# Kernel tuning notes

Measured on AMD Instinct MI355X. Metric: run time of the kernel, lower is better.

The kernel has to match this reference:

```python
import jax, jax.numpy as jnp
import numpy as np

N, E, B = 100000, 1600000, 64
IN, HID, OUT, ED = 64, 128, 128, 2
K, ALPHA = 16, 0.1
LN_EPS = 1e-5


def setup_inputs() -> dict:
    key = jax.random.key(0)
    ks = jax.random.split(key, 24)
    def gl(k, shape, fan_in):
        return jax.random.uniform(k, shape, jnp.float32, -1.0, 1.0) / np.sqrt(fan_in)
    inp = {
        "x": jax.random.normal(ks[0], (N, IN), jnp.float32),
        "edge_index": jax.random.randint(ks[1], (2, E), 0, N, jnp.int64),
        "batch": jnp.sort(jax.random.randint(ks[2], (N,), 0, B, jnp.int64)),
        "edge_attr": jax.random.normal(ks[3], (E, ED), jnp.float32),
        # conv1: edge lin (ED->IN) + mlp (IN->HID->HID)
        "We1": gl(ks[4], (ED, IN), ED), "be1": jnp.zeros((IN,)),
        "W1a": gl(ks[5], (IN, HID), IN), "b1a": jnp.zeros((HID,)),
        "W1b": gl(ks[6], (HID, HID), HID), "b1b": jnp.zeros((HID,)),
        "g1": jnp.ones((HID,)), "bn1": jnp.zeros((HID,)),
        # conv2: edge lin (ED->HID) + mlp (HID->OUT->OUT)
        "We2": gl(ks[7], (ED, HID), ED), "be2": jnp.zeros((HID,)),
        "W2a": gl(ks[8], (HID, OUT), HID), "b2a": jnp.zeros((OUT,)),
        "W2b": gl(ks[9], (OUT, OUT), OUT), "b2b": jnp.zeros((OUT,)),
        "g2": jnp.ones((OUT,)), "bn2": jnp.zeros((OUT,)),
        # gate nn (OUT -> OUT//2 -> 1)
        "Wg1": gl(ks[10], (OUT, OUT // 2), OUT), "bg1": jnp.zeros((OUT // 2,)),
        "Wg2": gl(ks[11], (OUT // 2, 1), OUT // 2), "bg2": jnp.zeros((1,)),
    }
    return inp


def _gelu(x):
    return jax.nn.gelu(x, approximate=False)


def _layernorm(x, g, b):
    mu = jnp.mean(x, axis=-1, keepdims=True)
    var = jnp.mean(jnp.square(x - mu), axis=-1, keepdims=True)
    return (x - mu) * jax.lax.rsqrt(var + LN_EPS) * g + b


def _gine(x, src, dst, edge_attr, We, be, W1, b1, W2, b2):
    # message: ReLU(x_j + lin(edge_attr)), aggregated by sum at dst; eps=0
    m = jax.nn.relu(x[src] + edge_attr @ We + be)          # [E, d]
    agg = jax.ops.segment_sum(m, dst, num_segments=N)      # [N, d]
    h = x + agg
    return _gelu(h @ W1 + b1) @ W2 + b2


def _appnp(x, src, dst):
    # gcn_norm with self-loops: deg_i = 1 + in-degree
    deg = jax.ops.segment_sum(jnp.ones((E,), x.dtype), dst, num_segments=N) + 1.0
    dis = jax.lax.rsqrt(deg)
    w = dis[src] * dis[dst]            # [E]
    selfw = 1.0 / deg                  # [N]
    def step(i, h):
        prop = jax.ops.segment_sum(w[:, None] * h[src], dst, num_segments=N) \
               + selfw[:, None] * h
        return (1.0 - ALPHA) * prop + ALPHA * x
    return jax.lax.fori_loop(0, K, step, x)


def reference(x, edge_index, batch, edge_attr,
              We1, be1, W1a, b1a, W1b, b1b, g1, bn1,
              We2, be2, W2a, b2a, W2b, b2b, g2, bn2,
              Wg1, bg1, Wg2, bg2):
    src, dst = edge_index[0], edge_index[1]
    h = _gine(x, src, dst, edge_attr, We1, be1, W1a, b1a, W1b, b1b)
    h = _layernorm(_gelu(h), g1, bn1)
    # dropout is identity in eval
    h = _gine(h, src, dst, edge_attr, We2, be2, W2a, b2a, W2b, b2b)
    h = _layernorm(h, g2, bn2)
    h = _appnp(h, src, dst)
    # attentional aggregation: per-graph softmax over gate scores
    gate = (_gelu(h @ Wg1 + bg1) @ Wg2 + bg2)[:, 0]        # [N]
    m = jax.ops.segment_max(gate, batch, num_segments=B)    # [B]
    e = jnp.exp(gate - m[batch])
    s = jax.ops.segment_sum(e, batch, num_segments=B)
    a = e / s[batch]
    g = jax.ops.segment_sum(a[:, None] * h, batch, num_segments=B)  # [B, OUT]
    return h, g
```

## Files before the change

### kernel.cpp

```cpp
#include <hip/hip_runtime.h>
#include <math.h>

#define N_NODES 100000
#define N_EDGES 1600000
#define N_B 64
#define D_IN 64
#define D_HID 128
#define D_OUT 128
#define K_ITER 16
#define LN_EPS 1e-5f

typedef short s8v __attribute__((ext_vector_type(8)));
typedef float f4v __attribute__((ext_vector_type(4)));

__device__ __forceinline__ float gelu_f(float x) {
    return 0.5f * x * (1.0f + erff(0.70710678118654752440f * x));
}

__device__ __forceinline__ float ubx(unsigned u) { return __uint_as_float(u << 16); }
__device__ __forceinline__ float uby(unsigned u) { return __uint_as_float(u & 0xffff0000u); }

__device__ __forceinline__ unsigned short bf_rne(float x) {
    unsigned u = __float_as_uint(x);
    u += 0x7fffu + ((u >> 16) & 1u);
    return (unsigned short)(u >> 16);
}
__device__ __forceinline__ float bf_f(unsigned short s) {
    return __uint_as_float(((unsigned)s) << 16);
}
__device__ __forceinline__ unsigned pack_bf2(float a, float b) {
    return (unsigned)bf_rne(a) | (((unsigned)bf_rne(b)) << 16);
}


__global__ __launch_bounds__(256) void hist_kernel(const int* __restrict__ dst, int* __restrict__ counts) {
    int e = blockIdx.x * 256 + threadIdx.x;
    if (e < N_EDGES) atomicAdd(&counts[dst[e]], 1);
}

__global__ __launch_bounds__(256) void deg_kernel(const int* __restrict__ counts,
                                                  float* __restrict__ dis, float* __restrict__ selfw,
                                                  float* __restrict__ rsq) {
    int i = blockIdx.x * 256 + threadIdx.x;
    if (i < N_NODES) {
        float d = (float)(counts[i] + 1);
        dis[i] = 1.0f / sqrtf(d);
        selfw[i] = 1.0f / d;
        rsq[i] = sqrtf(d);
    }
}

__global__ __launch_bounds__(1024) void scan1(const int* __restrict__ counts, int* __restrict__ rp,
                                              int* __restrict__ bsum) {
    __shared__ int tmp[1024];
    int t = threadIdx.x;
    int idx = blockIdx.x * 1024 + t;
    int v = (idx < N_NODES) ? counts[idx] : 0;
    tmp[t] = v;
    __syncthreads();
    for (int o = 1; o < 1024; o <<= 1) {
        int add = (t >= o) ? tmp[t - o] : 0;
        __syncthreads();
        tmp[t] += add;
        __syncthreads();
    }
    if (idx < N_NODES) rp[idx] = tmp[t] - v;
    if (t == 1023) bsum[blockIdx.x] = tmp[t];
}

__global__ void scan2(int* bsum, int nb) {
    if (threadIdx.x == 0 && blockIdx.x == 0) {
        int acc = 0;
        for (int i = 0; i < nb; i++) { int v = bsum[i]; bsum[i] = acc; acc += v; }
    }
}

__global__ __launch_bounds__(1024) void scan3(int* __restrict__ rp, const int* __restrict__ bsum,
                                              int* __restrict__ cursor) {
    int t = threadIdx.x;
    int idx = blockIdx.x * 1024 + t;
    if (idx < N_NODES) {
        int v = rp[idx] + bsum[blockIdx.x];
        rp[idx] = v;
        cursor[idx] = v;
    }
    if (idx == 0) rp[N_NODES] = N_EDGES;
}

__global__ __launch_bounds__(256) void scatter_kernel(const int* __restrict__ src, const int* __restrict__ dst,
                                                      const float* __restrict__ ea,
                                                      int* __restrict__ cursor, int4* __restrict__ edata) {
    int e = blockIdx.x * 256 + threadIdx.x;
    if (e >= N_EDGES) return;
    int s = src[e], d = dst[e];
    int pos = atomicAdd(&cursor[d], 1);
    float2 e2 = ((const float2*)ea)[e];
    int4 v;
    v.x = s;
    v.y = __float_as_int(e2.x);
    v.z = __float_as_int(e2.y);
    v.w = 0;
    edata[pos] = v;
}

__global__ __launch_bounds__(256) void split_kernel(const int4* __restrict__ edata, int* __restrict__ esrc) {
    int e = blockIdx.x * 256 + threadIdx.x;
    if (e < N_EDGES) esrc[e] = edata[e].x;
}

__global__ __launch_bounds__(256) void x_to_bf(const float4* __restrict__ x4, uint2* __restrict__ xb2) {
    int i = blockIdx.x * 256 + threadIdx.x;
    if (i < N_NODES * 16) {
        float4 v = x4[i];
        uint2 o;
        o.x = pack_bf2(v.x, v.y);
        o.y = pack_bf2(v.z, v.w);
        xb2[i] = o;
    }
}


__global__ __launch_bounds__(256) void conv1_gather(const float* __restrict__ x,
                                                    const unsigned short* __restrict__ xb,
                                                    const int* __restrict__ rp,
                                                    const int4* __restrict__ edata,
                                                    const float* __restrict__ We1, const float* __restrict__ be1,
                                                    float* __restrict__ out) {
    int gw = (blockIdx.x * 256 + threadIdx.x) >> 6;
    if (gw >= N_NODES) return;
    int lane = threadIdx.x & 63;
    float w0 = We1[lane], w1 = We1[64 + lane], bb = be1[lane];
    float acc = x[(size_t)gw * 64 + lane];
    int j = rp[gw], jend = rp[gw + 1];
    for (; j + 8 <= jend; j += 8) {
        int4 e0 = edata[j], e1 = edata[j + 1], e2 = edata[j + 2], e3 = edata[j + 3];
        int4 e4 = edata[j + 4], e5 = edata[j + 5], e6 = edata[j + 6], e7 = edata[j + 7];
        unsigned short v0 = xb[(size_t)e0.x * 64 + lane];
        unsigned short v1 = xb[(size_t)e1.x * 64 + lane];
        unsigned short v2 = xb[(size_t)e2.x * 64 + lane];
        unsigned short v3 = xb[(size_t)e3.x * 64 + lane];
        unsigned short v4 = xb[(size_t)e4.x * 64 + lane];
        unsigned short v5 = xb[(size_t)e5.x * 64 + lane];
        unsigned short v6 = xb[(size_t)e6.x * 64 + lane];
        unsigned short v7 = xb[(size_t)e7.x * 64 + lane];
        acc += fmaxf(bf_f(v0) + __int_as_float(e0.y) * w0 + __int_as_float(e0.z) * w1 + bb, 0.0f);
        acc += fmaxf(bf_f(v1) + __int_as_float(e1.y) * w0 + __int_as_float(e1.z) * w1 + bb, 0.0f);
        acc += fmaxf(bf_f(v2) + __int_as_float(e2.y) * w0 + __int_as_float(e2.z) * w1 + bb, 0.0f);
        acc += fmaxf(bf_f(v3) + __int_as_float(e3.y) * w0 + __int_as_float(e3.z) * w1 + bb, 0.0f);
        acc += fmaxf(bf_f(v4) + __int_as_float(e4.y) * w0 + __int_as_float(e4.z) * w1 + bb, 0.0f);
        acc += fmaxf(bf_f(v5) + __int_as_float(e5.y) * w0 + __int_as_float(e5.z) * w1 + bb, 0.0f);
        acc += fmaxf(bf_f(v6) + __int_as_float(e6.y) * w0 + __int_as_float(e6.z) * w1 + bb, 0.0f);
        acc += fmaxf(bf_f(v7) + __int_as_float(e7.y) * w0 + __int_as_float(e7.z) * w1 + bb, 0.0f);
    }
    for (; j < jend; j++) {
        int4 e = edata[j];
        unsigned short v = xb[(size_t)e.x * 64 + lane];
        acc += fmaxf(bf_f(v) + __int_as_float(e.y) * w0 + __int_as_float(e.z) * w1 + bb, 0.0f);
    }
    out[(size_t)gw * 64 + lane] = acc;
}

__global__ __launch_bounds__(256) void conv2_gather(const float* __restrict__ h1f, const unsigned* __restrict__ h1b,
                                                    const int* __restrict__ rp,
                                                    const int4* __restrict__ edata,
                                                    const float* __restrict__ We2, const float* __restrict__ be2,
                                                    float* __restrict__ out) {
    int gw = (blockIdx.x * 256 + threadIdx.x) >> 6;
    if (gw >= N_NODES) return;
    int lane = threadIdx.x & 63;
    int f0 = lane * 2;
    float w00 = We2[f0], w01 = We2[f0 + 1];
    float w10 = We2[128 + f0], w11 = We2[128 + f0 + 1];
    float b0 = be2[f0], b1 = be2[f0 + 1];
    float2 hc = ((const float2*)h1f)[(size_t)gw * 64 + lane];
    float a0 = hc.x, a1 = hc.y;
    int j = rp[gw], jend = rp[gw + 1];
    for (; j + 8 <= jend; j += 8) {
        int4 e0 = edata[j], e1 = edata[j + 1], e2 = edata[j + 2], e3 = edata[j + 3];
        int4 e4 = edata[j + 4], e5 = edata[j + 5], e6 = edata[j + 6], e7 = edata[j + 7];
        unsigned v0 = h1b[(size_t)e0.x * 64 + lane];
        unsigned v1 = h1b[(size_t)e1.x * 64 + lane];
        unsigned v2 = h1b[(size_t)e2.x * 64 + lane];
        unsigned v3 = h1b[(size_t)e3.x * 64 + lane];
        unsigned v4 = h1b[(size_t)e4.x * 64 + lane];
        unsigned v5 = h1b[(size_t)e5.x * 64 + lane];
        unsigned v6 = h1b[(size_t)e6.x * 64 + lane];
        unsigned v7 = h1b[(size_t)e7.x * 64 + lane];
        a0 += fmaxf(ubx(v0) + __int_as_float(e0.y) * w00 + __int_as_float(e0.z) * w10 + b0, 0.0f);
        a1 += fmaxf(uby(v0) + __int_as_float(e0.y) * w01 + __int_as_float(e0.z) * w11 + b1, 0.0f);
        a0 += fmaxf(ubx(v1) + __int_as_float(e1.y) * w00 + __int_as_float(e1.z) * w10 + b0, 0.0f);
        a1 += fmaxf(uby(v1) + __int_as_float(e1.y) * w01 + __int_as_float(e1.z) * w11 + b1, 0.0f);
        a0 += fmaxf(ubx(v2) + __int_as_float(e2.y) * w00 + __int_as_float(e2.z) * w10 + b0, 0.0f);
        a1 += fmaxf(uby(v2) + __int_as_float(e2.y) * w01 + __int_as_float(e2.z) * w11 + b1, 0.0f);
        a0 += fmaxf(ubx(v3) + __int_as_float(e3.y) * w00 + __int_as_float(e3.z) * w10 + b0, 0.0f);
        a1 += fmaxf(uby(v3) + __int_as_float(e3.y) * w01 + __int_as_float(e3.z) * w11 + b1, 0.0f);
        a0 += fmaxf(ubx(v4) + __int_as_float(e4.y) * w00 + __int_as_float(e4.z) * w10 + b0, 0.0f);
        a1 += fmaxf(uby(v4) + __int_as_float(e4.y) * w01 + __int_as_float(e4.z) * w11 + b1, 0.0f);
        a0 += fmaxf(ubx(v5) + __int_as_float(e5.y) * w00 + __int_as_float(e5.z) * w10 + b0, 0.0f);
        a1 += fmaxf(uby(v5) + __int_as_float(e5.y) * w01 + __int_as_float(e5.z) * w11 + b1, 0.0f);
        a0 += fmaxf(ubx(v6) + __int_as_float(e6.y) * w00 + __int_as_float(e6.z) * w10 + b0, 0.0f);
        a1 += fmaxf(uby(v6) + __int_as_float(e6.y) * w01 + __int_as_float(e6.z) * w11 + b1, 0.0f);
        a0 += fmaxf(ubx(v7) + __int_as_float(e7.y) * w00 + __int_as_float(e7.z) * w10 + b0, 0.0f);
        a1 += fmaxf(uby(v7) + __int_as_float(e7.y) * w01 + __int_as_float(e7.z) * w11 + b1, 0.0f);
    }
    for (; j < jend; j++) {
        int4 e = edata[j];
        unsigned v = h1b[(size_t)e.x * 64 + lane];
        a0 += fmaxf(ubx(v) + __int_as_float(e.y) * w00 + __int_as_float(e.z) * w10 + b0, 0.0f);
        a1 += fmaxf(uby(v) + __int_as_float(e.y) * w01 + __int_as_float(e.z) * w11 + b1, 0.0f);
    }
    out[(size_t)gw * 128 + f0] = a0;
    out[(size_t)gw * 128 + f0 + 1] = a1;
}


template <int Kd, bool GELU, bool LN, int OMODE, bool SCALE>
__global__ __launch_bounds__(256) void mlp_mfma(const float* __restrict__ A, const float* __restrict__ W,
                                                const float* __restrict__ bias, const float* __restrict__ g,
                                                const float* __restrict__ bn, float* __restrict__ outf,
                                                unsigned short* __restrict__ outb,
                                                const float* __restrict__ uscale) {
    __shared__ unsigned short sHi[8192];
    __shared__ unsigned short sLo[8192];
    int wave = threadIdx.x >> 6, lane = threadIdx.x & 63;
    int quad = lane >> 4, n = lane & 15;
    int rowA = blockIdx.x * 64 + wave * 16 + n;
    int rowAc = (rowA < N_NODES) ? rowA : 0;

    f4v acc[8];
    #pragma unroll
    for (int t = 0; t < 8; t++) acc[t] = (f4v){0.f, 0.f, 0.f, 0.f};

    for (int ph = 0; ph < Kd / 64; ph++) {
        __syncthreads();
        for (int idx = threadIdx.x; idx < 8192; idx += 256) {
            int k = idx >> 7, c = idx & 127;
            float v = W[(size_t)(ph * 64 + k) * 128 + c];
            unsigned short hi = bf_rne(v);
            unsigned short lo = bf_rne(v - bf_f(hi));
            int kk = k >> 5, q = (k >> 3) & 3, j = k & 7, t = c >> 4, nn = c & 15;
            int lidx = ((((kk * 4 + q) * 8 + t) * 16 + nn) << 3) + j;
            sHi[lidx] = hi;
            sLo[lidx] = lo;
        }
        __syncthreads();
        #pragma unroll
        for (int kk = 0; kk < 2; kk++) {
            int k0 = ph * 64 + kk * 32 + quad * 8;
            const float4* ap = (const float4*)(A + (size_t)rowAc * Kd + k0);
            float4 a0 = ap[0], a1 = ap[1];
            float av[8] = {a0.x, a0.y, a0.z, a0.w, a1.x, a1.y, a1.z, a1.w};
            s8v ahi, alo;
            #pragma unroll
            for (int j = 0; j < 8; j++) {
                unsigned short h = bf_rne(av[j]);
                ahi[j] = (short)h;
                alo[j] = (short)bf_rne(av[j] - bf_f(h));
            }
            int base = ((kk * 4 + quad) * 8) * 128;
            #pragma unroll
            for (int t = 0; t < 8; t++) {
                s8v bhi = *(const s8v*)&sHi[base + ((t * 16 + n) << 3)];
                s8v blo = *(const s8v*)&sLo[base + ((t * 16 + n) << 3)];
                acc[t] = __builtin_amdgcn_mfma_f32_16x16x32_bf16(ahi, bhi, acc[t], 0, 0, 0);
                acc[t] = __builtin_amdgcn_mfma_f32_16x16x32_bf16(ahi, blo, acc[t], 0, 0, 0);
                acc[t] = __builtin_amdgcn_mfma_f32_16x16x32_bf16(alo, bhi, acc[t], 0, 0, 0);
            }
        }
    }

    float bcol[8], gcol[8], bncol[8];
    #pragma unroll
    for (int t = 0; t < 8; t++) {
        bcol[t] = bias[t * 16 + n];
        if (LN) { gcol[t] = g[t * 16 + n]; bncol[t] = bn[t * 16 + n]; }
    }
    #pragma unroll
    for (int r = 0; r < 4; r++) {
        int row = blockIdx.x * 64 + wave * 16 + quad * 4 + r;
        float v[8];
        #pragma unroll
        for (int t = 0; t < 8; t++) {
            float x = acc[t][r] + bcol[t];
            v[t] = GELU ? gelu_f(x) : x;
        }
        if (LN) {
            float s = 0.f, q2 = 0.f;
            #pragma unroll
            for (int t = 0; t < 8; t++) { s += v[t]; q2 += v[t] * v[t]; }
            #pragma unroll
            for (int m = 1; m <= 8; m <<= 1) {
                s += __shfl_xor(s, m, 64);
                q2 += __shfl_xor(q2, m, 64);
            }
            float mu = s * (1.0f / 128.0f);
            float rs = rsqrtf(q2 * (1.0f / 128.0f) - mu * mu + LN_EPS);
            #pragma unroll
            for (int t = 0; t < 8; t++) v[t] = (v[t] - mu) * rs * gcol[t] + bncol[t];
        }
        if (row < N_NODES) {
            float us = SCALE ? uscale[row] : 1.0f;
            #pragma unroll
            for (int t = 0; t < 8; t++) {
                if (OMODE != 2) outf[(size_t)row * 128 + t * 16 + n] = v[t];
                if (OMODE >= 1) outb[(size_t)row * 128 + t * 16 + n] = bf_rne(SCALE ? v[t] * us : v[t]);
            }
        }
    }
}


__global__ __launch_bounds__(256) void gate_mfma(const float* __restrict__ h, const float* __restrict__ Wg1,
                                                 const float* __restrict__ bg1, const float* __restrict__ Wg2,
                                                 const float* __restrict__ bg2, float* __restrict__ gate) {
    __shared__ unsigned short sHi[8192];
    __shared__ unsigned short sLo[8192];
    int wave = threadIdx.x >> 6, lane = threadIdx.x & 63;
    int quad = lane >> 4, n = lane & 15;
    for (int idx = threadIdx.x; idx < 8192; idx += 256) {
        int k = idx >> 6, c = idx & 63;
        float v = Wg1[k * 64 + c];
        unsigned short hi = bf_rne(v);
        unsigned short lo = bf_rne(v - bf_f(hi));
        int kk = k >> 5, q = (k >> 3) & 3, j = k & 7, t = c >> 4, nn = c & 15;
        int lidx = ((((kk * 4 + q) * 4 + t) * 16 + nn) << 3) + j;
        sHi[lidx] = hi;
        sLo[lidx] = lo;
    }
    __syncthreads();
    int rowA = blockIdx.x * 64 + wave * 16 + n;
    int rowAc = (rowA < N_NODES) ? rowA : 0;
    f4v acc[4];
    #pragma unroll
    for (int t = 0; t < 4; t++) acc[t] = (f4v){0.f, 0.f, 0.f, 0.f};
    #pragma unroll
    for (int kk = 0; kk < 4; kk++) {
        const float4* ap = (const float4*)(h + (size_t)rowAc * 128 + kk * 32 + quad * 8);
        float4 a0 = ap[0], a1 = ap[1];
        float av[8] = {a0.x, a0.y, a0.z, a0.w, a1.x, a1.y, a1.z, a1.w};
        s8v ahi, alo;
        #pragma unroll
        for (int j = 0; j < 8; j++) {
            unsigned short hh = bf_rne(av[j]);
            ahi[j] = (short)hh;
            alo[j] = (short)bf_rne(av[j] - bf_f(hh));
        }
        int base = ((kk * 4 + quad) * 4) * 128;
        #pragma unroll
        for (int t = 0; t < 4; t++) {
            s8v bhi = *(const s8v*)&sHi[base + ((t * 16 + n) << 3)];
            s8v blo = *(const s8v*)&sLo[base + ((t * 16 + n) << 3)];
            acc[t] = __builtin_amdgcn_mfma_f32_16x16x32_bf16(ahi, bhi, acc[t], 0, 0, 0);
            acc[t] = __builtin_amdgcn_mfma_f32_16x16x32_bf16(ahi, blo, acc[t], 0, 0, 0);
            acc[t] = __builtin_amdgcn_mfma_f32_16x16x32_bf16(alo, bhi, acc[t], 0, 0, 0);
        }
    }
    float b2 = bg2[0];
    float bb[4], vv[4];
    #pragma unroll
    for (int t = 0; t < 4; t++) { bb[t] = bg1[t * 16 + n]; vv[t] = Wg2[t * 16 + n]; }
    #pragma unroll
    for (int r = 0; r < 4; r++) {
        int row = blockIdx.x * 64 + wave * 16 + quad * 4 + r;
        float val = 0.f;
        #pragma unroll
        for (int t = 0; t < 4; t++) val += gelu_f(acc[t][r] + bb[t]) * vv[t];
        #pragma unroll
        for (int m = 1; m <= 8; m <<= 1) val += __shfl_xor(val, m, 64);
        if (n == 0 && row < N_NODES) gate[row] = val + b2;
    }
}


template <bool LAST>
__global__ __launch_bounds__(256) void appnp_step_u(const unsigned* __restrict__ hin,
                                                    const unsigned* __restrict__ anchor,
                                                    unsigned* __restrict__ hout, float2* __restrict__ houtf,
                                                    const int* __restrict__ rp, const int* __restrict__ esrc,
                                                    const float* __restrict__ selfw,
                                                    const float* __restrict__ rsq) {
    int gw = (blockIdx.x * 256 + threadIdx.x) >> 6;
    if (gw >= N_NODES) return;
    int lane = threadIdx.x & 63;
    size_t idx = (size_t)gw * 64 + lane;
    unsigned hcp = hin[idx];
    float ax = ubx(hcp), ay = uby(hcp);
    int j = rp[gw], jend = rp[gw + 1];
    for (; j + 8 <= jend; j += 8) {
        int s0 = esrc[j],     s1 = esrc[j + 1], s2 = esrc[j + 2], s3 = esrc[j + 3];
        int s4 = esrc[j + 4], s5 = esrc[j + 5], s6 = esrc[j + 6], s7 = esrc[j + 7];
        unsigned v0 = hin[(size_t)s0 * 64 + lane];
        unsigned v1 = hin[(size_t)s1 * 64 + lane];
        unsigned v2 = hin[(size_t)s2 * 64 + lane];
        unsigned v3 = hin[(size_t)s3 * 64 + lane];
        unsigned v4 = hin[(size_t)s4 * 64 + lane];
        unsigned v5 = hin[(size_t)s5 * 64 + lane];
        unsigned v6 = hin[(size_t)s6 * 64 + lane];
        unsigned v7 = hin[(size_t)s7 * 64 + lane];
        ax += ubx(v0); ay += uby(v0);
        ax += ubx(v1); ay += uby(v1);
        ax += ubx(v2); ay += uby(v2);
        ax += ubx(v3); ay += uby(v3);
        ax += ubx(v4); ay += uby(v4);
        ax += ubx(v5); ay += uby(v5);
        ax += ubx(v6); ay += uby(v6);
        ax += ubx(v7); ay += uby(v7);
    }
    for (; j + 4 <= jend; j += 4) {
        int s0 = esrc[j], s1 = esrc[j + 1], s2 = esrc[j + 2], s3 = esrc[j + 3];
        unsigned v0 = hin[(size_t)s0 * 64 + lane];
        unsigned v1 = hin[(size_t)s1 * 64 + lane];
        unsigned v2 = hin[(size_t)s2 * 64 + lane];
        unsigned v3 = hin[(size_t)s3 * 64 + lane];
        ax += ubx(v0); ay += uby(v0);
        ax += ubx(v1); ay += uby(v1);
        ax += ubx(v2); ay += uby(v2);
        ax += ubx(v3); ay += uby(v3);
    }
    for (; j < jend; j++) {
        int s = esrc[j];
        unsigned v = hin[(size_t)s * 64 + lane];
        ax += ubx(v); ay += uby(v);
    }
    float swi = 0.9f * selfw[gw];
    unsigned ancp = anchor[idx];
    float ox = fmaf(swi, ax, 0.1f * ubx(ancp));
    float oy = fmaf(swi, ay, 0.1f * uby(ancp));
    if (LAST) {
        float rq = rsq[gw];
        float2 o; o.x = ox * rq; o.y = oy * rq;
        houtf[idx] = o;
    } else {
        hout[idx] = pack_bf2(ox, oy);
    }
}


__global__ void seg_begin(const int* __restrict__ batch, int* __restrict__ gbeg) {
    int b = threadIdx.x;
    if (b > N_B) return;
    if (b == N_B) { gbeg[N_B] = N_NODES; return; }
    int lo = 0, hi = N_NODES;
    while (lo < hi) {
        int mid = (lo + hi) >> 1;
        if (batch[mid] < b) lo = mid + 1; else hi = mid;
    }
    gbeg[b] = lo;
}

__global__ __launch_bounds__(256) void seg_max(const float* __restrict__ gate, const int* __restrict__ gbeg,
                                               float* __restrict__ gmax) {
    int b = blockIdx.x;
    int s = gbeg[b], e = gbeg[b + 1];
    float m = -INFINITY;
    for (int i = s + threadIdx.x; i < e; i += 256) m = fmaxf(m, gate[i]);
    for (int o = 32; o > 0; o >>= 1) m = fmaxf(m, __shfl_xor(m, o, 64));
    __shared__ float red[4];
    if ((threadIdx.x & 63) == 0) red[threadIdx.x >> 6] = m;
    __syncthreads();
    if (threadIdx.x == 0) gmax[b] = fmaxf(fmaxf(red[0], red[1]), fmaxf(red[2], red[3]));
}

__global__ __launch_bounds__(256) void seg_sum(const float* __restrict__ gate, const int* __restrict__ gbeg,
                                               const float* __restrict__ gmax, float* __restrict__ gsum) {
    int b = blockIdx.x;
    int s = gbeg[b], e = gbeg[b + 1];
    float m = gmax[b];
    float acc = 0.0f;
    for (int i = s + threadIdx.x; i < e; i += 256) acc += expf(gate[i] - m);
    for (int o = 32; o > 0; o >>= 1) acc += __shfl_xor(acc, o, 64);
    __shared__ float red[4];
    if ((threadIdx.x & 63) == 0) red[threadIdx.x >> 6] = acc;
    __syncthreads();
    if (threadIdx.x == 0) gsum[b] = red[0] + red[1] + red[2] + red[3];
}

__global__ __launch_bounds__(512) void seg_pool(const float* __restrict__ h, const float* __restrict__ gate,
                                                const int* __restrict__ gbeg, const float* __restrict__ gmax,
                                                const float* __restrict__ gsum, float* __restrict__ gout) {
    int b = blockIdx.x >> 3, slice = blockIdx.x & 7;
    int team = threadIdx.x >> 7;
    int f = threadIdx.x & 127;
    int s = gbeg[b], e = gbeg[b + 1];
    float m = gmax[b];
    float inv = (e > s) ? 1.0f / gsum[b] : 0.0f;
    float acc = 0.0f;
    for (int i = s + slice * 4 + team; i < e; i += 32) {
        float a = expf(gate[i] - m) * inv;
        acc = fmaf(a, h[(size_t)i * 128 + f], acc);
    }
    __shared__ float red[4][128];
    red[team][f] = acc;
    __syncthreads();
    if (team == 0) {
        float v = red[0][f] + red[1][f] + red[2][f] + red[3][f];
        atomicAdd(&gout[b * 128 + f], v);
    }
}


extern "C" void kernel_launch(void* const* d_in, const int* in_sizes, int n_in,
                              void* d_out, int out_size, void* d_ws, size_t ws_size,
                              hipStream_t stream) {
    const float* x     = (const float*)d_in[0];
    const int*   ei    = (const int*)d_in[1];
    const int*   batch = (const int*)d_in[2];
    const float* ea    = (const float*)d_in[3];
    const float* We1 = (const float*)d_in[4];
    const float* be1 = (const float*)d_in[5];
    const float* W1a = (const float*)d_in[6];
    const float* b1a = (const float*)d_in[7];
    const float* W1b = (const float*)d_in[8];
    const float* b1b = (const float*)d_in[9];
    const float* g1  = (const float*)d_in[10];
    const float* bn1 = (const float*)d_in[11];
    const float* We2 = (const float*)d_in[12];
    const float* be2 = (const float*)d_in[13];
    const float* W2a = (const float*)d_in[14];
    const float* b2a = (const float*)d_in[15];
    const float* W2b = (const float*)d_in[16];
    const float* b2b = (const float*)d_in[17];
    const float* g2  = (const float*)d_in[18];
    const float* bn2 = (const float*)d_in[19];
    const float* Wg1 = (const float*)d_in[20];
    const float* bg1 = (const float*)d_in[21];
    const float* Wg2 = (const float*)d_in[22];
    const float* bg2 = (const float*)d_in[23];

    float* outH = (float*)d_out;
    float* outG = outH + (size_t)N_NODES * 128;

    char* w = (char*)d_ws;
    auto carve = [&](size_t bytes) {
        void* p = (void*)w;
        w += ((bytes + 255) / 256) * 256;
        return p;
    };
    float*  bufB   = (float*)carve((size_t)N_NODES * 128 * 4);
    float*  bufC   = (float*)carve((size_t)N_NODES * 128 * 4);
    int4*   edata  = (int4*)carve((size_t)N_EDGES * 16);
    int*    counts = (int*)carve((size_t)N_NODES * 4);
    int*    rp     = (int*)carve((size_t)(N_NODES + 1) * 4);
    int*    cursor = (int*)carve((size_t)N_NODES * 4);
    float*  dis    = (float*)carve((size_t)N_NODES * 4);
    float*  selfw  = (float*)carve((size_t)N_NODES * 4);
    float*  rsq    = (float*)carve((size_t)N_NODES * 4);
    float*  gate   = (float*)carve((size_t)N_NODES * 4);
    int*    bsum   = (int*)carve(128 * 4);
    float*  gmax   = (float*)carve(N_B * 4);
    float*  gsum   = (float*)carve(N_B * 4);
    int*    gbeg   = (int*)carve((N_B + 1) * 4);

    const int* src = ei;
    const int* dst = ei + N_EDGES;

    const int NB_SCAN = (N_NODES + 1023) / 1024;
    const int EB = (N_EDGES + 255) / 256;
    const int NBLK = (N_NODES + 255) / 256;
    const int WBLK = (N_NODES + 3) / 4;
    const int MBLK = (N_NODES + 63) / 64;

    unsigned short* h1bf  = (unsigned short*)bufC;
    unsigned* ancU  = (unsigned*)bufC;
    unsigned* pingA = ancU + (size_t)N_NODES * 64;
    unsigned* pingB = (unsigned*)bufB;
    unsigned short* xb = (unsigned short*)pingA;
    int*      esrc  = (int*)(bufB + (size_t)N_NODES * 64);

    hipMemsetAsync(counts, 0, (size_t)N_NODES * 4, stream);
    hist_kernel<<<EB, 256, 0, stream>>>(dst, counts);
    deg_kernel<<<NBLK, 256, 0, stream>>>(counts, dis, selfw, rsq);
    scan1<<<NB_SCAN, 1024, 0, stream>>>(counts, rp, bsum);
    scan2<<<1, 64, 0, stream>>>(bsum, NB_SCAN);
    scan3<<<NB_SCAN, 1024, 0, stream>>>(rp, bsum, cursor);
    scatter_kernel<<<EB, 256, 0, stream>>>(src, dst, ea, cursor, edata);
    x_to_bf<<<(N_NODES * 16 + 255) / 256, 256, 0, stream>>>((const float4*)x, (uint2*)xb);

    conv1_gather<<<WBLK, 256, 0, stream>>>(x, xb, rp, edata, We1, be1, bufB);
    mlp_mfma<64, true, false, 0, false><<<MBLK, 256, 0, stream>>>(bufB, W1a, b1a, nullptr, nullptr, outH, nullptr, nullptr);
    mlp_mfma<128, true, true, 1, false><<<MBLK, 256, 0, stream>>>(outH, W1b, b1b, g1, bn1, bufB, h1bf, nullptr);

    conv2_gather<<<WBLK, 256, 0, stream>>>(bufB, (const unsigned*)h1bf, rp, edata, We2, be2, outH);
    mlp_mfma<128, true, false, 0, false><<<MBLK, 256, 0, stream>>>(outH, W2a, b2a, nullptr, nullptr, bufB, nullptr, nullptr);
    mlp_mfma<128, false, true, 2, true><<<MBLK, 256, 0, stream>>>(bufB, W2b, b2b, g2, bn2, nullptr, (unsigned short*)ancU, dis);

    split_kernel<<<EB, 256, 0, stream>>>(edata, esrc);

    const unsigned* cur = ancU;
    for (int k = 1; k <= K_ITER - 1; k++) {
        unsigned* dstbuf = (k & 1) ? pingA : pingB;
        appnp_step_u<false><<<WBLK, 256, 0, stream>>>(cur, ancU, dstbuf, nullptr, rp, esrc, selfw, nullptr);
        cur = dstbuf;
    }
    appnp_step_u<true><<<WBLK, 256, 0, stream>>>(cur, ancU, nullptr, (float2*)outH, rp, esrc, selfw, rsq);

    gate_mfma<<<MBLK, 256, 0, stream>>>(outH, Wg1, bg1, Wg2, bg2, gate);
    seg_begin<<<1, 128, 0, stream>>>(batch, gbeg);
    seg_max<<<N_B, 256, 0, stream>>>(gate, gbeg, gmax);
    seg_sum<<<N_B, 256, 0, stream>>>(gate, gbeg, gmax, gsum);
    hipMemsetAsync(outG, 0, (size_t)N_B * 128 * 4, stream);
    seg_pool<<<N_B * 8, 512, 0, stream>>>(outH, gate, gbeg, gmax, gsum, outG);
}
```

Before: 1.779 ms.

## Gather multiple edges per wave with 16-byte row loads and shuffle reduction

The per-node gather kernels (conv1, conv2, and the APPNP step) now split each 64-lane wave into sub-groups. Each lane loads a 16-byte chunk of a neighbour row, so several edges are processed in parallel instead of each lane loading a 2- or 4-byte element per edge. Partial sums are combined across sub-groups with xor shuffles, and only the first lanes write the row with vector stores. The aim is fewer, wider memory transactions and more edges in flight per wave. The cost is extra shuffle reductions, more registers, and idle lanes during the tail and the final write.

New measurement: 1.832 ms. 3.0% more time.

```diff
diff --git a/kernel.cpp b/kernel.cpp
--- a/kernel.cpp
+++ b/kernel.cpp
@@ -121,7 +121,7 @@
 
 
 __global__ __launch_bounds__(256) void conv1_gather(const float* __restrict__ x,
-                                                    const unsigned short* __restrict__ xb,
+                                                    const unsigned* __restrict__ xb,
                                                     const int* __restrict__ rp,
                                                     const int4* __restrict__ edata,
                                                     const float* __restrict__ We1, const float* __restrict__ be1,
@@ -129,35 +129,70 @@
     int gw = (blockIdx.x * 256 + threadIdx.x) >> 6;
     if (gw >= N_NODES) return;
     int lane = threadIdx.x & 63;
-    float w0 = We1[lane], w1 = We1[64 + lane], bb = be1[lane];
-    float acc = x[(size_t)gw * 64 + lane];
+    int oct = lane >> 3;
+    int sl = lane & 7;
+    float w0c[8], w1c[8], bc[8];
+    #pragma unroll
+    for (int t = 0; t < 8; t++) {
+        int col = sl * 8 + t;
+        w0c[t] = We1[col];
+        w1c[t] = We1[64 + col];
+        bc[t] = be1[col];
+    }
+    float a[8];
+    #pragma unroll
+    for (int t = 0; t < 8; t++) a[t] = 0.f;
+
+#define C1ACC(E, V)                                                              \
+    {                                                                            \
+        float eax = __int_as_float((E).y), eay = __int_as_float((E).z);          \
+        a[0] += fmaxf(ubx((V).x) + eax * w0c[0] + eay * w1c[0] + bc[0], 0.f);    \
+        a[1] += fmaxf(uby((V).x) + eax * w0c[1] + eay * w1c[1] + bc[1], 0.f);    \
+        a[2] += fmaxf(ubx((V).y) + eax * w0c[2] + eay * w1c[2] + bc[2], 0.f);    \
+        a[3] += fmaxf(uby((V).y) + eax * w0c[3] + eay * w1c[3] + bc[3], 0.f);    \
+        a[4] += fmaxf(ubx((V).z) + eax * w0c[4] + eay * w1c[4] + bc[4], 0.f);    \
+        a[5] += fmaxf(uby((V).z) + eax * w0c[5] + eay * w1c[5] + bc[5], 0.f);    \
+        a[6] += fmaxf(ubx((V).w) + eax * w0c[6] + eay * w1c[6] + bc[6], 0.f);    \
+        a[7] += fmaxf(uby((V).w) + eax * w0c[7] + eay * w1c[7] + bc[7], 0.f);    \
+    }
+
     int j = rp[gw], jend = rp[gw + 1];
+    for (; j + 16 <= jend; j += 16) {
+        int4 e0 = edata[j + oct];
+        int4 e1 = edata[j + 8 + oct];
+        uint4 v0 = *((const uint4*)(xb + (size_t)e0.x * 32) + sl);
+        uint4 v1 = *((const uint4*)(xb + (size_t)e1.x * 32) + sl);
+        C1ACC(e0, v0);
+        C1ACC(e1, v1);
+    }
     for (; j + 8 <= jend; j += 8) {
-        int4 e0 = edata[j], e1 = edata[j + 1], e2 = edata[j + 2], e3 = edata[j + 3];
-        int4 e4 = edata[j + 4], e5 = edata[j + 5], e6 = edata[j + 6], e7 = edata[j + 7];
-        unsigned short v0 = xb[(size_t)e0.x * 64 + lane];
-        unsigned short v1 = xb[(size_t)e1.x * 64 + lane];
-        unsigned short v2 = xb[(size_t)e2.x * 64 + lane];
-        unsigned short v3 = xb[(size_t)e3.x * 64 + lane];
-        unsigned short v4 = xb[(size_t)e4.x * 64 + lane];
-        unsigned short v5 = xb[(size_t)e5.x * 64 + lane];
-        unsigned short v6 = xb[(size_t)e6.x * 64 + lane];
-        unsigned short v7 = xb[(size_t)e7.x * 64 + lane];
-        acc += fmaxf(bf_f(v0) + __int_as_float(e0.y) * w0 + __int_as_float(e0.z) * w1 + bb, 0.0f);
-        acc += fmaxf(bf_f(v1) + __int_as_float(e1.y) * w0 + __int_as_float(e1.z) * w1 + bb, 0.0f);
-        acc += fmaxf(bf_f(v2) + __int_as_float(e2.y) * w0 + __int_as_float(e2.z) * w1 + bb, 0.0f);
-        acc += fmaxf(bf_f(v3) + __int_as_float(e3.y) * w0 + __int_as_float(e3.z) * w1 + bb, 0.0f);
-        acc += fmaxf(bf_f(v4) + __int_as_float(e4.y) * w0 + __int_as_float(e4.z) * w1 + bb, 0.0f);
-        acc += fmaxf(bf_f(v5) + __int_as_float(e5.y) * w0 + __int_as_float(e5.z) * w1 + bb, 0.0f);
-        acc += fmaxf(bf_f(v6) + __int_as_float(e6.y) * w0 + __int_as_float(e6.z) * w1 + bb, 0.0f);
-        acc += fmaxf(bf_f(v7) + __int_as_float(e7.y) * w0 + __int_as_float(e7.z) * w1 + bb, 0.0f);
-    }
-    for (; j < jend; j++) {
-        int4 e = edata[j];
-        unsigned short v = xb[(size_t)e.x * 64 + lane];
-        acc += fmaxf(bf_f(v) + __int_as_float(e.y) * w0 + __int_as_float(e.z) * w1 + bb, 0.0f);
-    }
-    out[(size_t)gw * 64 + lane] = acc;
+        int4 e0 = edata[j + oct];
+        uint4 v0 = *((const uint4*)(xb + (size_t)e0.x * 32) + sl);
+        C1ACC(e0, v0);
+    }
+    int rem = jend - j;
+    if (rem > 0) {
+        int4 e0 = edata[j + ((oct < rem) ? oct : 0)];
+        uint4 v0 = *((const uint4*)(xb + (size_t)e0.x * 32) + sl);
+        if (oct < rem) C1ACC(e0, v0);
+    }
+#undef C1ACC
+    #pragma unroll
+    for (int t = 0; t < 8; t++) {
+        a[t] += __shfl_xor(a[t], 8, 64);
+        a[t] += __shfl_xor(a[t], 16, 64);
+        a[t] += __shfl_xor(a[t], 32, 64);
+    }
+    if (lane < 8) {
+        const float4* xr = (const float4*)(x + (size_t)gw * 64);
+        float4 s0 = xr[sl * 2], s1 = xr[sl * 2 + 1];
+        float4* orow = (float4*)(out + (size_t)gw * 64);
+        float4 o0, o1;
+        o0.x = a[0] + s0.x; o0.y = a[1] + s0.y; o0.z = a[2] + s0.z; o0.w = a[3] + s0.w;
+        o1.x = a[4] + s1.x; o1.y = a[5] + s1.y; o1.z = a[6] + s1.z; o1.w = a[7] + s1.w;
+        orow[sl * 2] = o0;
+        orow[sl * 2 + 1] = o1;
+    }
 }
 
 __global__ __launch_bounds__(256) void conv2_gather(const float* __restrict__ h1f, const unsigned* __restrict__ h1b,
@@ -168,49 +203,83 @@
     int gw = (blockIdx.x * 256 + threadIdx.x) >> 6;
     if (gw >= N_NODES) return;
     int lane = threadIdx.x & 63;
-    int f0 = lane * 2;
-    float w00 = We2[f0], w01 = We2[f0 + 1];
-    float w10 = We2[128 + f0], w11 = We2[128 + f0 + 1];
-    float b0 = be2[f0], b1 = be2[f0 + 1];
-    float2 hc = ((const float2*)h1f)[(size_t)gw * 64 + lane];
-    float a0 = hc.x, a1 = hc.y;
+    int quad = lane >> 4;
+    int sl = lane & 15;
+    float w0c[8], w1c[8], bc[8];
+    #pragma unroll
+    for (int t = 0; t < 8; t++) {
+        int col = sl * 8 + t;
+        w0c[t] = We2[col];
+        w1c[t] = We2[128 + col];
+        bc[t] = be2[col];
+    }
+    float a[8];
+    #pragma unroll
+    for (int t = 0; t < 8; t++) a[t] = 0.f;
+
+#define C2ACC(E, V)                                                              \
+    {                                                                            \
+        float eax = __int_as_float((E).y), eay = __int_as_float((E).z);          \
+        a[0] += fmaxf(ubx((V).x) + eax * w0c[0] + eay * w1c[0] + bc[0], 0.f);    \
+        a[1] += fmaxf(uby((V).x) + eax * w0c[1] + eay * w1c[1] + bc[1], 0.f);    \
+        a[2] += fmaxf(ubx((V).y) + eax * w0c[2] + eay * w1c[2] + bc[2], 0.f);    \
+        a[3] += fmaxf(uby((V).y) + eax * w0c[3] + eay * w1c[3] + bc[3], 0.f);    \
+        a[4] += fmaxf(ubx((V).z) + eax * w0c[4] + eay * w1c[4] + bc[4], 0.f);    \
+        a[5] += fmaxf(uby((V).z) + eax * w0c[5] + eay * w1c[5] + bc[5], 0.f);    \
+        a[6] += fmaxf(ubx((V).w) + eax * w0c[6] + eay * w1c[6] + bc[6], 0.f);    \
+        a[7] += fmaxf(uby((V).w) + eax * w0c[7] + eay * w1c[7] + bc[7], 0.f);    \
+    }
+
     int j = rp[gw], jend = rp[gw + 1];
+    for (; j + 16 <= jend; j += 16) {
+        int4 e0 = edata[j + quad];
+        int4 e1 = edata[j + 4 + quad];
+        int4 e2 = edata[j + 8 + quad];
+        int4 e3 = edata[j + 12 + quad];
+        uint4 v0 = *((const uint4*)(h1b + (size_t)e0.x * 64) + sl);
+        uint4 v1 = *((const uint4*)(h1b + (size_t)e1.x * 64) + sl);
+        uint4 v2 = *((const uint4*)(h1b + (size_t)e2.x * 64) + sl);
+        uint4 v3 = *((const uint4*)(h1b + (size_t)e3.x * 64) + sl);
+        C2ACC(e0, v0);
+        C2ACC(e1, v1);
+        C2ACC(e2, v2);
+        C2ACC(e3, v3);
+    }
     for (; j + 8 <= jend; j += 8) {
-        int4 e0 = edata[j], e1 = edata[j + 1], e2 = edata[j + 2], e3 = edata[j + 3];
-        int4 e4 = edata[j + 4], e5 = edata[j + 5], e6 = edata[j + 6], e7 = edata[j + 7];
-        unsigned v0 = h1b[(size_t)e0.x * 64 + lane];
-        unsigned v1 = h1b[(size_t)e1.x * 64 + lane];
-        unsigned v2 = h1b[(size_t)e2.x * 64 + lane];
-        unsigned v3 = h1b[(size_t)e3.x * 64 + lane];
-        unsigned v4 = h1b[(size_t)e4.x * 64 + lane];
-        unsigned v5 = h1b[(size_t)e5.x * 64 + lane];
-        unsigned v6 = h1b[(size_t)e6.x * 64 + lane];
-        unsigned v7 = h1b[(size_t)e7.x * 64 + lane];
-        a0 += fmaxf(ubx(v0) + __int_as_float(e0.y) * w00 + __int_as_float(e0.z) * w10 + b0, 0.0f);
-        a1 += fmaxf(uby(v0) + __int_as_float(e0.y) * w01 + __int_as_float(e0.z) * w11 + b1, 0.0f);
-        a0 += fmaxf(ubx(v1) + __int_as_float(e1.y) * w00 + __int_as_float(e1.z) * w10 + b0, 0.0f);
-        a1 += fmaxf(uby(v1) + __int_as_float(e1.y) * w01 + __int_as_float(e1.z) * w11 + b1, 0.0f);
-        a0 += fmaxf(ubx(v2) + __int_as_float(e2.y) * w00 + __int_as_float(e2.z) * w10 + b0, 0.0f);
-        a1 += fmaxf(uby(v2) + __int_as_float(e2.y) * w01 + __int_as_float(e2.z) * w11 + b1, 0.0f);
-        a0 += fmaxf(ubx(v3) + __int_as_float(e3.y) * w00 + __int_as_float(e3.z) * w10 + b0, 0.0f);
-        a1 += fmaxf(uby(v3) + __int_as_float(e3.y) * w01 + __int_as_float(e3.z) * w11 + b1, 0.0f);
-        a0 += fmaxf(ubx(v4) + __int_as_float(e4.y) * w00 + __int_as_float(e4.z) * w10 + b0, 0.0f);
-        a1 += fmaxf(uby(v4) + __int_as_float(e4.y) * w01 + __int_as_float(e4.z) * w11 + b1, 0.0f);
-        a0 += fmaxf(ubx(v5) + __int_as_float(e5.y) * w00 + __int_as_float(e5.z) * w10 + b0, 0.0f);
-        a1 += fmaxf(uby(v5) + __int_as_float(e5.y) * w01 + __int_as_float(e5.z) * w11 + b1, 0.0f);
-        a0 += fmaxf(ubx(v6) + __int_as_float(e6.y) * w00 + __int_as_float(e6.z) * w10 + b0, 0.0f);
-        a1 += fmaxf(uby(v6) + __int_as_float(e6.y) * w01 + __int_as_float(e6.z) * w11 + b1, 0.0f);
-        a0 += fmaxf(ubx(v7) + __int_as_float(e7.y) * w00 + __int_as_float(e7.z) * w10 + b0, 0.0f);
-        a1 += fmaxf(uby(v7) + __int_as_float(e7.y) * w01 + __int_as_float(e7.z) * w11 + b1, 0.0f);
-    }
-    for (; j < jend; j++) {
-        int4 e = edata[j];
-        unsigned v = h1b[(size_t)e.x * 64 + lane];
-        a0 += fmaxf(ubx(v) + __int_as_float(e.y) * w00 + __int_as_float(e.z) * w10 + b0, 0.0f);
-        a1 += fmaxf(uby(v) + __int_as_float(e.y) * w01 + __int_as_float(e.z) * w11 + b1, 0.0f);
-    }
-    out[(size_t)gw * 128 + f0] = a0;
-    out[(size_t)gw * 128 + f0 + 1] = a1;
+        int4 e0 = edata[j + quad];
+        int4 e1 = edata[j + 4 + quad];
+        uint4 v0 = *((const uint4*)(h1b + (size_t)e0.x * 64) + sl);
+        uint4 v1 = *((const uint4*)(h1b + (size_t)e1.x * 64) + sl);
+        C2ACC(e0, v0);
+        C2ACC(e1, v1);
+    }
+    for (; j + 4 <= jend; j += 4) {
+        int4 e0 = edata[j + quad];
+        uint4 v0 = *((const uint4*)(h1b + (size_t)e0.x * 64) + sl);
+        C2ACC(e0, v0);
+    }
+    int rem = jend - j;
+    if (rem > 0) {
+        int4 e0 = edata[j + ((quad < rem) ? quad : 0)];
+        uint4 v0 = *((const uint4*)(h1b + (size_t)e0.x * 64) + sl);
+        if (quad < rem) C2ACC(e0, v0);
+    }
+#undef C2ACC
+    #pragma unroll
+    for (int t = 0; t < 8; t++) {
+        a[t] += __shfl_xor(a[t], 16, 64);
+        a[t] += __shfl_xor(a[t], 32, 64);
+    }
+    if (lane < 16) {
+        const float4* hr = (const float4*)(h1f + (size_t)gw * 128);
+        float4 s0 = hr[sl * 2], s1 = hr[sl * 2 + 1];
+        float4* orow = (float4*)(out + (size_t)gw * 128);
+        float4 o0, o1;
+        o0.x = a[0] + s0.x; o0.y = a[1] + s0.y; o0.z = a[2] + s0.z; o0.w = a[3] + s0.w;
+        o1.x = a[4] + s1.x; o1.y = a[5] + s1.y; o1.z = a[6] + s1.z; o1.w = a[7] + s1.w;
+        orow[sl * 2] = o0;
+        orow[sl * 2 + 1] = o1;
+    }
 }
 
 
@@ -375,63 +444,98 @@
 template <bool LAST>
 __global__ __launch_bounds__(256) void appnp_step_u(const unsigned* __restrict__ hin,
                                                     const unsigned* __restrict__ anchor,
-                                                    unsigned* __restrict__ hout, float2* __restrict__ houtf,
+                                                    unsigned* __restrict__ hout, float* __restrict__ houtf,
                                                     const int* __restrict__ rp, const int* __restrict__ esrc,
                                                     const float* __restrict__ selfw,
                                                     const float* __restrict__ rsq) {
     int gw = (blockIdx.x * 256 + threadIdx.x) >> 6;
     if (gw >= N_NODES) return;
     int lane = threadIdx.x & 63;
-    size_t idx = (size_t)gw * 64 + lane;
-    unsigned hcp = hin[idx];
-    float ax = ubx(hcp), ay = uby(hcp);
+    int quad = lane >> 4;
+    int sl = lane & 15;
+    float a[8];
+    #pragma unroll
+    for (int t = 0; t < 8; t++) a[t] = 0.f;
+
+#define UACC(V)                                   \
+    {                                             \
+        a[0] += ubx((V).x); a[1] += uby((V).x);   \
+        a[2] += ubx((V).y); a[3] += uby((V).y);   \
+        a[4] += ubx((V).z); a[5] += uby((V).z);   \
+        a[6] += ubx((V).w); a[7] += uby((V).w);   \
+    }
+
     int j = rp[gw], jend = rp[gw + 1];
+    for (; j + 16 <= jend; j += 16) {
+        int s0 = esrc[j + quad];
+        int s1 = esrc[j + 4 + quad];
+        int s2 = esrc[j + 8 + quad];
+        int s3 = esrc[j + 12 + quad];
+        uint4 v0 = *((const uint4*)(hin + (size_t)s0 * 64) + sl);
+        uint4 v1 = *((const uint4*)(hin + (size_t)s1 * 64) + sl);
+        uint4 v2 = *((const uint4*)(hin + (size_t)s2 * 64) + sl);
+        uint4 v3 = *((const uint4*)(hin + (size_t)s3 * 64) + sl);
+        UACC(v0);
+        UACC(v1);
+        UACC(v2);
+        UACC(v3);
+    }
     for (; j + 8 <= jend; j += 8) {
-        int s0 = esrc[j],     s1 = esrc[j + 1], s2 = esrc[j + 2], s3 = esrc[j + 3];
-        int s4 = esrc[j + 4], s5 = esrc[j + 5], s6 = esrc[j + 6], s7 = esrc[j + 7];
-        unsigned v0 = hin[(size_t)s0 * 64 + lane];
-        unsigned v1 = hin[(size_t)s1 * 64 + lane];
-        unsigned v2 = hin[(size_t)s2 * 64 + lane];
-        unsigned v3 = hin[(size_t)s3 * 64 + lane];
-        unsigned v4 = hin[(size_t)s4 * 64 + lane];
-        unsigned v5 = hin[(size_t)s5 * 64 + lane];
-        unsigned v6 = hin[(size_t)s6 * 64 + lane];
-        unsigned v7 = hin[(size_t)s7 * 64 + lane];
-        ax += ubx(v0); ay += uby(v0);
-        ax += ubx(v1); ay += uby(v1);
-        ax += ubx(v2); ay += uby(v2);
-        ax += ubx(v3); ay += uby(v3);
-        ax += ubx(v4); ay += uby(v4);
-        ax += ubx(v5); ay += uby(v5);
-        ax += ubx(v6); ay += uby(v6);
-        ax += ubx(v7); ay += uby(v7);
+        int s0 = esrc[j + quad];
+        int s1 = esrc[j + 4 + quad];
+        uint4 v0 = *((const uint4*)(hin + (size_t)s0 * 64) + sl);
+        uint4 v1 = *((const uint4*)(hin + (size_t)s1 * 64) + sl);
+        UACC(v0);
+        UACC(v1);
     }
     for (; j + 4 <= jend; j += 4) {
-        int s0 = esrc[j], s1 = esrc[j + 1], s2 = esrc[j + 2], s3 = esrc[j + 3];
-        unsigned v0 = hin[(size_t)s0 * 64 + lane];
-        unsigned v1 = hin[(size_t)s1 * 64 + lane];
-        unsigned v2 = hin[(size_t)s2 * 64 + lane];
-        unsigned v3 = hin[(size_t)s3 * 64 + lane];
-        ax += ubx(v0); ay += uby(v0);
-        ax += ubx(v1); ay += uby(v1);
-        ax += ubx(v2); ay += uby(v2);
-        ax += ubx(v3); ay += uby(v3);
-    }
-    for (; j < jend; j++) {
-        int s = esrc[j];
-        unsigned v = hin[(size_t)s * 64 + lane];
-        ax += ubx(v); ay += uby(v);
-    }
+        int s0 = esrc[j + quad];
+        uint4 v0 = *((const uint4*)(hin + (size_t)s0 * 64) + sl);
+        UACC(v0);
+    }
+    int rem = jend - j;
+    if (rem > 0) {
+        int s0 = esrc[j + ((quad < rem) ? quad : 0)];
+        uint4 v0 = *((const uint4*)(hin + (size_t)s0 * 64) + sl);
+        if (quad < rem) UACC(v0);
+    }
+#undef UACC
+    #pragma unroll
+    for (int t = 0; t < 8; t++) {
+        a[t] += __shfl_xor(a[t], 16, 64);
+        a[t] += __shfl_xor(a[t], 32, 64);
+    }
+    uint4 hc = *((const uint4*)(hin + (size_t)gw * 64) + sl);
+    uint4 an = *((const uint4*)(anchor + (size_t)gw * 64) + sl);
     float swi = 0.9f * selfw[gw];
-    unsigned ancp = anchor[idx];
-    float ox = fmaf(swi, ax, 0.1f * ubx(ancp));
-    float oy = fmaf(swi, ay, 0.1f * uby(ancp));
+    float o[8];
+    o[0] = fmaf(swi, a[0] + ubx(hc.x), 0.1f * ubx(an.x));
+    o[1] = fmaf(swi, a[1] + uby(hc.x), 0.1f * uby(an.x));
+    o[2] = fmaf(swi, a[2] + ubx(hc.y), 0.1f * ubx(an.y));
+    o[3] = fmaf(swi, a[3] + uby(hc.y), 0.1f * uby(an.y));
+    o[4] = fmaf(swi, a[4] + ubx(hc.z), 0.1f * ubx(an.z));
+    o[5] = fmaf(swi, a[5] + uby(hc.z), 0.1f * uby(an.z));
+    o[6] = fmaf(swi, a[6] + ubx(hc.w), 0.1f * ubx(an.w));
+    o[7] = fmaf(swi, a[7] + uby(hc.w), 0.1f * uby(an.w));
     if (LAST) {
-        float rq = rsq[gw];
-        float2 o; o.x = ox * rq; o.y = oy * rq;
-        houtf[idx] = o;
+        if (lane < 16) {
+            float rq = rsq[gw];
+            float4* orow = (float4*)(houtf + (size_t)gw * 128);
+            float4 w0, w1;
+            w0.x = o[0] * rq; w0.y = o[1] * rq; w0.z = o[2] * rq; w0.w = o[3] * rq;
+            w1.x = o[4] * rq; w1.y = o[5] * rq; w1.z = o[6] * rq; w1.w = o[7] * rq;
+            orow[sl * 2] = w0;
+            orow[sl * 2 + 1] = w1;
+        }
     } else {
-        hout[idx] = pack_bf2(ox, oy);
+        if (lane < 16) {
+            uint4 w;
+            w.x = pack_bf2(o[0], o[1]);
+            w.y = pack_bf2(o[2], o[3]);
+            w.z = pack_bf2(o[4], o[5]);
+            w.w = pack_bf2(o[6], o[7]);
+            *((uint4*)(hout + (size_t)gw * 64) + sl) = w;
+        }
     }
 }
 
@@ -576,7 +680,7 @@
     scatter_kernel<<<EB, 256, 0, stream>>>(src, dst, ea, cursor, edata);
     x_to_bf<<<(N_NODES * 16 + 255) / 256, 256, 0, stream>>>((const float4*)x, (uint2*)xb);
 
-    conv1_gather<<<WBLK, 256, 0, stream>>>(x, xb, rp, edata, We1, be1, bufB);
+    conv1_gather<<<WBLK, 256, 0, stream>>>(x, (const unsigned*)xb, rp, edata, We1, be1, bufB);
     mlp_mfma<64, true, false, 0, false><<<MBLK, 256, 0, stream>>>(bufB, W1a, b1a, nullptr, nullptr, outH, nullptr, nullptr);
     mlp_mfma<128, true, true, 1, false><<<MBLK, 256, 0, stream>>>(outH, W1b, b1b, g1, bn1, bufB, h1bf, nullptr);
 
@@ -592,7 +696,7 @@
         appnp_step_u<false><<<WBLK, 256, 0, stream>>>(cur, ancU, dstbuf, nullptr, rp, esrc, selfw, nullptr);
         cur = dstbuf;
     }
-    appnp_step_u<true><<<WBLK, 256, 0, stream>>>(cur, ancU, nullptr, (float2*)outH, rp, esrc, selfw, rsq);
+    appnp_step_u<true><<<WBLK, 256, 0, stream>>>(cur, ancU, nullptr, outH, rp, esrc, selfw, rsq);
 
     gate_mfma<<<MBLK, 256, 0, stream>>>(outH, Wg1, bg1, Wg2, bg2, gate);
     seg_begin<<<1, 128, 0, stream>>>(batch, gbeg);
```

## Replace random CSR scatter with two-pass bucketed binning scatter

Applied to the files above, without the earlier changes.

Replaces the single-pass scatter, which does one global atomic and one random 16-byte write per edge, with two passes. The first pass bins edges into coarse destination buckets of 512 nodes, using shared-memory histograms and one staged coalesced write per block. The second pass scatters each bucket into its final CSR position, so the atomics and writes fall in a small, cache-resident window. This aims to improve locality of the CSR build, at the cost of an extra pass over 1.6M records through a temp buffer aliased onto bufB.

Measured after the change: 1.754 ms. No clear change (-1.4%).

```diff
diff --git a/kernel.cpp b/kernel.cpp
--- a/kernel.cpp
+++ b/kernel.cpp
@@ -9,6 +9,12 @@
 #define D_OUT 128
 #define K_ITER 16
 #define LN_EPS 1e-5f
+
+#define BSH 9
+#define NBUCK 196
+#define NBUCK_PAD 200
+#define BSPLIT 4
+#define CHUNK 2048
 
 typedef short s8v __attribute__((ext_vector_type(8)));
 typedef float f4v __attribute__((ext_vector_type(4)));
@@ -87,20 +93,79 @@
     if (idx == 0) rp[N_NODES] = N_EDGES;
 }
 
-__global__ __launch_bounds__(256) void scatter_kernel(const int* __restrict__ src, const int* __restrict__ dst,
-                                                      const float* __restrict__ ea,
-                                                      int* __restrict__ cursor, int4* __restrict__ edata) {
-    int e = blockIdx.x * 256 + threadIdx.x;
-    if (e >= N_EDGES) return;
-    int s = src[e], d = dst[e];
-    int pos = atomicAdd(&cursor[d], 1);
-    float2 e2 = ((const float2*)ea)[e];
-    int4 v;
-    v.x = s;
-    v.y = __float_as_int(e2.x);
-    v.z = __float_as_int(e2.y);
-    v.w = 0;
-    edata[pos] = v;
+__global__ void binit(const int* __restrict__ rp, int* __restrict__ bcursor) {
+    int b = threadIdx.x;
+    if (b < NBUCK) bcursor[b] = rp[b << BSH];
+}
+
+__global__ __launch_bounds__(256) void bin_kernel(const int* __restrict__ src, const int* __restrict__ dst,
+                                                  const float* __restrict__ ea,
+                                                  int* __restrict__ bcursor, int4* __restrict__ tmp) {
+    __shared__ int hist[NBUCK];
+    __shared__ int loff[NBUCK];
+    __shared__ int gbase[NBUCK];
+    __shared__ int total_s;
+    __shared__ int4 stage[CHUNK];
+    int tid = threadIdx.x;
+    int base = blockIdx.x * CHUNK;
+    for (int t = tid; t < NBUCK; t += 256) hist[t] = 0;
+    __syncthreads();
+    int4 rec[8];
+    int bk[8], rk[8];
+    bool val[8];
+    #pragma unroll
+    for (int k = 0; k < 8; k++) {
+        int e = base + k * 256 + tid;
+        val[k] = (e < N_EDGES);
+        if (val[k]) {
+            int s = src[e], d = dst[e];
+            float2 e2 = ((const float2*)ea)[e];
+            rec[k].x = s;
+            rec[k].y = __float_as_int(e2.x);
+            rec[k].z = __float_as_int(e2.y);
+            rec[k].w = d;
+            bk[k] = d >> BSH;
+            rk[k] = atomicAdd(&hist[bk[k]], 1);
+        }
+    }
+    __syncthreads();
+    if (tid == 0) {
+        int acc = 0;
+        for (int b = 0; b < NBUCK; b++) { loff[b] = acc; acc += hist[b]; }
+        total_s = acc;
+    }
+    __syncthreads();
+    if (tid < NBUCK && hist[tid] > 0) gbase[tid] = atomicAdd(&bcursor[tid], hist[tid]);
+    __syncthreads();
+    #pragma unroll
+    for (int k = 0; k < 8; k++)
+        if (val[k]) stage[loff[bk[k]] + rk[k]] = rec[k];
+    __syncthreads();
+    int total = total_s;
+    for (int s = tid; s < total; s += 256) {
+        int lo = 0, hi = NBUCK - 1;
+        while (lo < hi) {
+            int mid = (lo + hi + 1) >> 1;
+            if (loff[mid] <= s) lo = mid; else hi = mid - 1;
+        }
+        tmp[gbase[lo] + (s - loff[lo])] = stage[s];
+    }
+}
+
+__global__ __launch_bounds__(256) void scatter2_kernel(const int4* __restrict__ tmp, const int* __restrict__ rp,
+                                                       int* __restrict__ cursor, int4* __restrict__ edata) {
+    int b = blockIdx.x % NBUCK_PAD;
+    int slice = blockIdx.x / NBUCK_PAD;
+    if (b >= NBUCK) return;
+    int lo = rp[b << BSH];
+    int nend = (b + 1) << BSH;
+    if (nend > N_NODES) nend = N_NODES;
+    int hi = rp[nend];
+    for (int i = lo + slice * 256 + threadIdx.x; i < hi; i += BSPLIT * 256) {
+        int4 r = tmp[i];
+        int pos = atomicAdd(&cursor[r.w], 1);
+        edata[pos] = r;
+    }
 }
 
 __global__ __launch_bounds__(256) void split_kernel(const int4* __restrict__ edata, int* __restrict__ esrc) {
@@ -547,6 +612,7 @@
     float*  rsq    = (float*)carve((size_t)N_NODES * 4);
     float*  gate   = (float*)carve((size_t)N_NODES * 4);
     int*    bsum   = (int*)carve(128 * 4);
+    int*    bcursor= (int*)carve(NBUCK_PAD * 4);
     float*  gmax   = (float*)carve(N_B * 4);
     float*  gsum   = (float*)carve(N_B * 4);
     int*    gbeg   = (int*)carve((N_B + 1) * 4);
@@ -559,6 +625,7 @@
     const int NBLK = (N_NODES + 255) / 256;
     const int WBLK = (N_NODES + 3) / 4;
     const int MBLK = (N_NODES + 63) / 64;
+    const int ABLK = (N_EDGES + CHUNK - 1) / CHUNK;
 
     unsigned short* h1bf  = (unsigned short*)bufC;
     unsigned* ancU  = (unsigned*)bufC;
@@ -566,6 +633,7 @@
     unsigned* pingB = (unsigned*)bufB;
     unsigned short* xb = (unsigned short*)pingA;
     int*      esrc  = (int*)(bufB + (size_t)N_NODES * 64);
+    int4*     tmp   = (int4*)bufB;
 
     hipMemsetAsync(counts, 0, (size_t)N_NODES * 4, stream);
     hist_kernel<<<EB, 256, 0, stream>>>(dst, counts);
@@ -573,7 +641,9 @@
     scan1<<<NB_SCAN, 1024, 0, stream>>>(counts, rp, bsum);
     scan2<<<1, 64, 0, stream>>>(bsum, NB_SCAN);
     scan3<<<NB_SCAN, 1024, 0, stream>>>(rp, bsum, cursor);
-    scatter_kernel<<<EB, 256, 0, stream>>>(src, dst, ea, cursor, edata);
+    binit<<<1, 256, 0, stream>>>(rp, bcursor);
+    bin_kernel<<<ABLK, 256, 0, stream>>>(src, dst, ea, bcursor, tmp);
+    scatter2_kernel<<<NBUCK_PAD * BSPLIT, 256, 0, stream>>>(tmp, rp, cursor, edata);
     x_to_bf<<<(N_NODES * 16 + 255) / 256, 256, 0, stream>>>((const float4*)x, (uint2*)xb);
 
     conv1_gather<<<WBLK, 256, 0, stream>>>(x, xb, rp, edata, We1, be1, bufB);
```
